# Optimization experiments

Measured on AMD Instinct MI355X. Metric: run time of the kernel, lower is better.

Reference implementation:

```python
import jax, jax.numpy as jnp
import numpy as np

B, S, D = 16, 2048, 768
NORM = 1.0 / float(np.sqrt(D))


def setup_inputs() -> dict:
    key = jax.random.key(0)
    k1, k2, k3, k4, k5 = jax.random.split(key, 5)
    b_in = jax.random.normal(k1, (B, S, D), dtype=jnp.float32)
    mask = jax.random.randint(k2, (B, S), 0, 2, dtype=jnp.int64)
    # row 0 must be unmasked: the module returns attention[:, 0, :], and a fully
    # masked query row softmaxes all -inf -> NaN (same quirk as the torch source).
    mask = mask.at[:, 0].set(1)
    Wq = jax.random.normal(k3, (D, D), dtype=jnp.float32) * 0.02
    Wk = jax.random.normal(k4, (D, D), dtype=jnp.float32) * 0.02
    Wv = jax.random.normal(k5, (D, D), dtype=jnp.float32) * 0.02
    return {"b_in": b_in, "mask": mask, "Wq": Wq, "Wk": Wk, "Wv": Wv}


def reference(b_in, mask, Wq, Wk, Wv):
    # nn.Linear(bias=False): y = x @ W.T  (W is [out, in])
    q = jnp.einsum("bsd,ed->bse", b_in, Wq)
    k = jnp.einsum("bsd,ed->bse", b_in, Wk)
    v = jnp.einsum("bsd,ed->bse", b_in, Wv)
    # full [B, S, S] score matrix, as in the original bmm
    scores = jnp.einsum("bqd,bkd->bqk", q, k) * NORM
    # mask.unsqueeze(2): [B, S, 1] broadcasts over the KEY axis -> masks whole query rows
    scores = jnp.where(mask[:, :, None] == 0, -jnp.inf, scores)
    attn = jax.nn.softmax(scores, axis=-1)
    out = jnp.einsum("bqk,bkd->bqd", attn, v)
    return out[:, 0, :]
```

## Files before the change

### kernel.cpp

```cpp
#include <hip/hip_runtime.h>
#include <math.h>

#define BB 16
#define SS 2048
#define DD 768

#define NORM_SCALE 0.036084391824351615f

#define ECH 24
#define EPC (DD / ECH)

__global__ void rowdot_kernel(const float* __restrict__ src, size_t src_stride,
                              const float* __restrict__ W,
                              float* __restrict__ dst, float scale,
                              float* __restrict__ zero_buf) {
    int wid  = blockIdx.x * 4 + (threadIdx.x >> 6);
    int lane = threadIdx.x & 63;
    int b = wid / DD;
    int e = wid % DD;
    const float4* xr = (const float4*)(src + (size_t)b * src_stride);
    const float4* wr = (const float4*)(W + (size_t)e * DD);
    float acc = 0.f;
#pragma unroll
    for (int k = 0; k < 3; ++k) {
        float4 xv = xr[lane + k * 64];
        float4 wv = wr[lane + k * 64];
        acc += xv.x * wv.x + xv.y * wv.y + xv.z * wv.z + xv.w * wv.w;
    }
#pragma unroll
    for (int off = 32; off > 0; off >>= 1) acc += __shfl_down(acc, off);
    if (lane == 0) dst[wid] = acc * scale;
    if (zero_buf != nullptr && lane == 1) zero_buf[wid] = 0.f;
}

__global__ void kq_split_kernel(const float* __restrict__ q0,
                                const float* __restrict__ Wk,
                                float* __restrict__ kqs) {
    __shared__ float qs[EPC];
    int echunk = blockIdx.x;
    int b      = blockIdx.y;
    int t      = threadIdx.x;
    if (t < EPC) qs[t] = q0[b * DD + echunk * EPC + t];
    __syncthreads();
    const float4* Wk4 = (const float4*)(Wk + (size_t)(echunk * EPC) * DD);
    float4 acc = {0.f, 0.f, 0.f, 0.f};
#pragma unroll 4
    for (int e = 0; e < EPC; ++e) {
        float q = qs[e];
        float4 w = Wk4[e * (DD / 4) + t];
        acc.x += q * w.x;
        acc.y += q * w.y;
        acc.z += q * w.z;
        acc.w += q * w.w;
    }
    float* dst = kqs + b * DD + t * 4;
    atomicAdd(dst + 0, acc.x);
    atomicAdd(dst + 1, acc.y);
    atomicAdd(dst + 2, acc.z);
    atomicAdd(dst + 3, acc.w);
}

__global__ void score_kernel(const float* __restrict__ x,
                             const float* __restrict__ kqs,
                             float* __restrict__ scores) {
    int wid  = blockIdx.x * 4 + (threadIdx.x >> 6);
    int lane = threadIdx.x & 63;
    int b = wid / SS;
    const float4* xr = (const float4*)(x + (size_t)wid * DD);
    const float4* kr = (const float4*)(kqs + b * DD);
    float acc = 0.f;
#pragma unroll
    for (int k = 0; k < 3; ++k) {
        float4 xv = xr[lane + k * 64];
        float4 kv = kr[lane + k * 64];
        acc += xv.x * kv.x + xv.y * kv.y + xv.z * kv.z + xv.w * kv.w;
    }
#pragma unroll
    for (int off = 32; off > 0; off >>= 1) acc += __shfl_down(acc, off);
    if (lane == 0) scores[wid] = acc;
}

__global__ void softmax_kernel(const float* __restrict__ scores,
                               float* __restrict__ attn,
                               float* __restrict__ c) {
    __shared__ float redm[4];
    __shared__ float reds[4];
    __shared__ float bcast[2];
    int b = blockIdx.x;
    int tid = threadIdx.x;
    int wave = tid >> 6, lane = tid & 63;

    for (int d = tid; d < DD; d += 256) c[b * DD + d] = 0.f;

    float v[8];
    float mx = -INFINITY;
#pragma unroll
    for (int i = 0; i < 8; ++i) {
        v[i] = scores[b * SS + tid + i * 256];
        mx = fmaxf(mx, v[i]);
    }
#pragma unroll
    for (int off = 32; off > 0; off >>= 1) mx = fmaxf(mx, __shfl_down(mx, off));
    if (lane == 0) redm[wave] = mx;
    __syncthreads();
    if (tid == 0) bcast[0] = fmaxf(fmaxf(redm[0], redm[1]), fmaxf(redm[2], redm[3]));
    __syncthreads();
    mx = bcast[0];

    float sum = 0.f;
#pragma unroll
    for (int i = 0; i < 8; ++i) {
        v[i] = expf(v[i] - mx);
        sum += v[i];
    }
#pragma unroll
    for (int off = 32; off > 0; off >>= 1) sum += __shfl_down(sum, off);
    if (lane == 0) reds[wave] = sum;
    __syncthreads();
    if (tid == 0) bcast[1] = 1.f / (reds[0] + reds[1] + reds[2] + reds[3]);
    __syncthreads();
    float inv = bcast[1];
#pragma unroll
    for (int i = 0; i < 8; ++i) attn[b * SS + tid + i * 256] = v[i] * inv;
}

__global__ void cacc_kernel(const float* __restrict__ x,
                            const float* __restrict__ attn,
                            float* __restrict__ c) {
    __shared__ float as[64];
    int chunk = blockIdx.x;
    int b     = blockIdx.y;
    int t     = threadIdx.x;
    const int ROWS = SS / 32;
    int s0 = chunk * ROWS;
    if (t < ROWS) as[t] = attn[b * SS + s0 + t];
    __syncthreads();
    const float4* xb = (const float4*)(x + ((size_t)b * SS + s0) * DD);
    float4 acc = {0.f, 0.f, 0.f, 0.f};
#pragma unroll 4
    for (int r = 0; r < ROWS; ++r) {
        float a = as[r];
        float4 xv = xb[r * (DD / 4) + t];
        acc.x += a * xv.x;
        acc.y += a * xv.y;
        acc.z += a * xv.z;
        acc.w += a * xv.w;
    }
    float* dst = c + b * DD + t * 4;
    atomicAdd(dst + 0, acc.x);
    atomicAdd(dst + 1, acc.y);
    atomicAdd(dst + 2, acc.z);
    atomicAdd(dst + 3, acc.w);
}

extern "C" void kernel_launch(void* const* d_in, const int* in_sizes, int n_in,
                              void* d_out, int out_size, void* d_ws, size_t ws_size,
                              hipStream_t stream) {
    const float* b_in = (const float*)d_in[0];
    const float* Wq = (const float*)d_in[2];
    const float* Wk = (const float*)d_in[3];
    const float* Wv = (const float*)d_in[4];
    float* out = (float*)d_out;

    float* ws     = (float*)d_ws;
    float* q0     = ws;
    float* kqs    = q0 + BB * DD;
    float* scores = kqs + BB * DD;
    float* attn   = scores + BB * SS;
    float* c      = attn + BB * SS;

    rowdot_kernel<<<BB * DD / 4, 256, 0, stream>>>(b_in, (size_t)SS * DD, Wq,
                                                   q0, NORM_SCALE, kqs);
    kq_split_kernel<<<dim3(ECH, BB), 192, 0, stream>>>(q0, Wk, kqs);
    score_kernel<<<BB * SS / 4, 256, 0, stream>>>(b_in, kqs, scores);
    softmax_kernel<<<BB, 256, 0, stream>>>(scores, attn, c);
    cacc_kernel<<<dim3(32, BB), 192, 0, stream>>>(b_in, attn, c);
    rowdot_kernel<<<BB * DD / 4, 256, 0, stream>>>(c, (size_t)DD, Wv, out,
                                                   1.f, nullptr);
}
```

Baseline: 195.4 us.

## Fuse score, softmax and weighted-sum into a split-softmax single pass over input

Replaces the separate score, softmax and attention-accumulate kernels with a flash-style kernel. Each block scores 16 rows, stages them in shared memory and emits a partial max, partial sum and partial weighted row. A small combine kernel then merges the partials per batch. The aim is to read the large input tensor once instead of twice and to drop the atomics, at the cost of a partial-output buffer of a few MB and a low-parallelism combine step with only 16 blocks.

```diff
diff --git a/kernel.cpp b/kernel.cpp
--- a/kernel.cpp
+++ b/kernel.cpp
@@ -9,6 +9,9 @@
 
 #define ECH 24
 #define EPC (DD / ECH)
+
+#define RPC 16
+#define NCH (SS / RPC)
 
 __global__ void rowdot_kernel(const float* __restrict__ src, size_t src_stride,
                               const float* __restrict__ W,
@@ -60,97 +63,119 @@
     atomicAdd(dst + 3, acc.w);
 }
 
-__global__ void score_kernel(const float* __restrict__ x,
+__global__ void flash_kernel(const float* __restrict__ x,
                              const float* __restrict__ kqs,
-                             float* __restrict__ scores) {
-    int wid  = blockIdx.x * 4 + (threadIdx.x >> 6);
-    int lane = threadIdx.x & 63;
-    int b = wid / SS;
-    const float4* xr = (const float4*)(x + (size_t)wid * DD);
+                             float* __restrict__ m_part,
+                             float* __restrict__ l_part,
+                             float* __restrict__ o_part) {
+    __shared__ float xs[RPC * DD];
+    __shared__ float sc[RPC];
+    __shared__ float p[RPC];
+    __shared__ float mbc[1];
+    int chunk = blockIdx.x;
+    int b     = blockIdx.y;
+    int tid   = threadIdx.x;
+    int wave  = tid >> 6, lane = tid & 63;
+    int s0    = chunk * RPC;
+
     const float4* kr = (const float4*)(kqs + b * DD);
-    float acc = 0.f;
-#pragma unroll
-    for (int k = 0; k < 3; ++k) {
-        float4 xv = xr[lane + k * 64];
-        float4 kv = kr[lane + k * 64];
-        acc += xv.x * kv.x + xv.y * kv.y + xv.z * kv.z + xv.w * kv.w;
-    }
-#pragma unroll
-    for (int off = 32; off > 0; off >>= 1) acc += __shfl_down(acc, off);
-    if (lane == 0) scores[wid] = acc;
-}
-
-__global__ void softmax_kernel(const float* __restrict__ scores,
-                               float* __restrict__ attn,
+    float4 kf0 = kr[lane];
+    float4 kf1 = kr[lane + 64];
+    float4 kf2 = kr[lane + 128];
+
+#pragma unroll
+    for (int j = 0; j < 4; ++j) {
+        int r = wave * 4 + j;
+        const float4* xr = (const float4*)(x + ((size_t)b * SS + s0 + r) * DD);
+        float4 x0 = xr[lane];
+        float4 x1 = xr[lane + 64];
+        float4 x2 = xr[lane + 128];
+        float4* xsr = (float4*)(xs + r * DD);
+        xsr[lane]       = x0;
+        xsr[lane + 64]  = x1;
+        xsr[lane + 128] = x2;
+        float acc = x0.x * kf0.x + x0.y * kf0.y + x0.z * kf0.z + x0.w * kf0.w
+                  + x1.x * kf1.x + x1.y * kf1.y + x1.z * kf1.z + x1.w * kf1.w
+                  + x2.x * kf2.x + x2.y * kf2.y + x2.z * kf2.z + x2.w * kf2.w;
+#pragma unroll
+        for (int off = 32; off > 0; off >>= 1) acc += __shfl_down(acc, off);
+        if (lane == 0) sc[r] = acc;
+    }
+    __syncthreads();
+
+    if (tid == 0) {
+        float m = sc[0];
+#pragma unroll
+        for (int r = 1; r < RPC; ++r) m = fmaxf(m, sc[r]);
+        mbc[0] = m;
+    }
+    __syncthreads();
+    if (tid < RPC) p[tid] = expf(sc[tid] - mbc[0]);
+    __syncthreads();
+
+    float a0 = 0.f, a1 = 0.f, a2 = 0.f;
+#pragma unroll
+    for (int r = 0; r < RPC; ++r) {
+        float pr = p[r];
+        a0 += pr * xs[r * DD + tid];
+        a1 += pr * xs[r * DD + tid + 256];
+        a2 += pr * xs[r * DD + tid + 512];
+    }
+    int pidx = b * NCH + chunk;
+    float* op = o_part + (size_t)pidx * DD;
+    op[tid]       = a0;
+    op[tid + 256] = a1;
+    op[tid + 512] = a2;
+    if (tid == 0) {
+        float l = 0.f;
+#pragma unroll
+        for (int r = 0; r < RPC; ++r) l += p[r];
+        m_part[pidx] = mbc[0];
+        l_part[pidx] = l;
+    }
+}
+
+__global__ void combine_kernel(const float* __restrict__ m_part,
+                               const float* __restrict__ l_part,
+                               const float* __restrict__ o_part,
                                float* __restrict__ c) {
-    __shared__ float redm[4];
-    __shared__ float reds[4];
-    __shared__ float bcast[2];
+    __shared__ float w[NCH];
+    __shared__ float bc[2];
     int b = blockIdx.x;
     int tid = threadIdx.x;
-    int wave = tid >> 6, lane = tid & 63;
-
-    for (int d = tid; d < DD; d += 256) c[b * DD + d] = 0.f;
-
-    float v[8];
-    float mx = -INFINITY;
-#pragma unroll
-    for (int i = 0; i < 8; ++i) {
-        v[i] = scores[b * SS + tid + i * 256];
-        mx = fmaxf(mx, v[i]);
-    }
-#pragma unroll
-    for (int off = 32; off > 0; off >>= 1) mx = fmaxf(mx, __shfl_down(mx, off));
-    if (lane == 0) redm[wave] = mx;
-    __syncthreads();
-    if (tid == 0) bcast[0] = fmaxf(fmaxf(redm[0], redm[1]), fmaxf(redm[2], redm[3]));
-    __syncthreads();
-    mx = bcast[0];
-
-    float sum = 0.f;
-#pragma unroll
-    for (int i = 0; i < 8; ++i) {
-        v[i] = expf(v[i] - mx);
-        sum += v[i];
-    }
-#pragma unroll
-    for (int off = 32; off > 0; off >>= 1) sum += __shfl_down(sum, off);
-    if (lane == 0) reds[wave] = sum;
-    __syncthreads();
-    if (tid == 0) bcast[1] = 1.f / (reds[0] + reds[1] + reds[2] + reds[3]);
-    __syncthreads();
-    float inv = bcast[1];
-#pragma unroll
-    for (int i = 0; i < 8; ++i) attn[b * SS + tid + i * 256] = v[i] * inv;
-}
-
-__global__ void cacc_kernel(const float* __restrict__ x,
-                            const float* __restrict__ attn,
-                            float* __restrict__ c) {
-    __shared__ float as[64];
-    int chunk = blockIdx.x;
-    int b     = blockIdx.y;
-    int t     = threadIdx.x;
-    const int ROWS = SS / 32;
-    int s0 = chunk * ROWS;
-    if (t < ROWS) as[t] = attn[b * SS + s0 + t];
-    __syncthreads();
-    const float4* xb = (const float4*)(x + ((size_t)b * SS + s0) * DD);
-    float4 acc = {0.f, 0.f, 0.f, 0.f};
+
+    if (tid < NCH) w[tid] = m_part[b * NCH + tid];
+    __syncthreads();
+    if (tid == 0) {
+        float M = w[0];
+        for (int i = 1; i < NCH; ++i) M = fmaxf(M, w[i]);
+        bc[0] = M;
+    }
+    __syncthreads();
+    float M = bc[0];
+    if (tid < NCH) w[tid] = expf(w[tid] - M);
+    __syncthreads();
+    if (tid == 0) {
+        float l = 0.f;
+        for (int i = 0; i < NCH; ++i) l += w[i] * l_part[b * NCH + i];
+        bc[1] = 1.f / l;
+    }
+    __syncthreads();
+    float inv = bc[1];
+
+    float a0 = 0.f, a1 = 0.f, a2 = 0.f;
+    const float* op = o_part + (size_t)b * NCH * DD;
 #pragma unroll 4
-    for (int r = 0; r < ROWS; ++r) {
-        float a = as[r];
-        float4 xv = xb[r * (DD / 4) + t];
-        acc.x += a * xv.x;
-        acc.y += a * xv.y;
-        acc.z += a * xv.z;
-        acc.w += a * xv.w;
-    }
-    float* dst = c + b * DD + t * 4;
-    atomicAdd(dst + 0, acc.x);
-    atomicAdd(dst + 1, acc.y);
-    atomicAdd(dst + 2, acc.z);
-    atomicAdd(dst + 3, acc.w);
+    for (int cc = 0; cc < NCH; ++cc) {
+        float wc = w[cc];
+        const float* o = op + (size_t)cc * DD;
+        a0 += wc * o[tid];
+        a1 += wc * o[tid + 256];
+        a2 += wc * o[tid + 512];
+    }
+    c[b * DD + tid]       = a0 * inv;
+    c[b * DD + tid + 256] = a1 * inv;
+    c[b * DD + tid + 512] = a2 * inv;
 }
 
 extern "C" void kernel_launch(void* const* d_in, const int* in_sizes, int n_in,
@@ -165,16 +190,17 @@
     float* ws     = (float*)d_ws;
     float* q0     = ws;
     float* kqs    = q0 + BB * DD;
-    float* scores = kqs + BB * DD;
-    float* attn   = scores + BB * SS;
-    float* c      = attn + BB * SS;
+    float* m_part = kqs + BB * DD;
+    float* l_part = m_part + BB * NCH;
+    float* o_part = l_part + BB * NCH;
+    float* c      = o_part + (size_t)BB * NCH * DD;
 
     rowdot_kernel<<<BB * DD / 4, 256, 0, stream>>>(b_in, (size_t)SS * DD, Wq,
                                                    q0, NORM_SCALE, kqs);
     kq_split_kernel<<<dim3(ECH, BB), 192, 0, stream>>>(q0, Wk, kqs);
-    score_kernel<<<BB * SS / 4, 256, 0, stream>>>(b_in, kqs, scores);
-    softmax_kernel<<<BB, 256, 0, stream>>>(scores, attn, c);
-    cacc_kernel<<<dim3(32, BB), 192, 0, stream>>>(b_in, attn, c);
+    flash_kernel<<<dim3(NCH, BB), 256, 0, stream>>>(b_in, kqs,
+                                                    m_part, l_part, o_part);
+    combine_kernel<<<BB, 256, 0, stream>>>(m_part, l_part, o_part, c);
     rowdot_kernel<<<BB * DD / 4, 256, 0, stream>>>(c, (size_t)DD, Wv, out,
                                                    1.f, nullptr);
 }
```

Result: faster. 191.3 us (-2.1%).
